# Performance work log

Measured on AMD Instinct MI355X. Metric: run time of the kernel, lower is better.

## Reference

```python
import jax, jax.numpy as jnp
import numpy as np

NT, NB, NC = 64, 1024, 512
H, E, NCLS = 512, 128, 97


def gru_cell(x, h, w_ih, w_hh, b_ih, b_hh):
    # torch.nn.GRUCell semantics; gate order r, z, n
    gi = x @ w_ih.T + b_ih
    gh = h @ w_hh.T + b_hh
    ir, iz, inn = jnp.split(gi, 3, axis=1)
    hr, hz, hn = jnp.split(gh, 3, axis=1)
    r = jax.nn.sigmoid(ir + hr)
    z = jax.nn.sigmoid(iz + hz)
    n = jnp.tanh(inn + r * hn)
    return (1.0 - z) * n + z * h


def setup_inputs() -> dict:
    key = jax.random.key(0)
    ks = jax.random.split(key, 12)
    s = 0.02
    return {
        'feats': jax.random.normal(ks[0], (NT, NB, NC), jnp.float32),
        'w_i2h': jax.random.normal(ks[1], (H, NC), jnp.float32) * s,
        'w_h2h': jax.random.normal(ks[2], (H, H), jnp.float32) * s,
        'b_h2h': jnp.zeros((H,), jnp.float32),
        'w_score': jax.random.normal(ks[3], (1, H), jnp.float32) * s,
        'w_ih': jax.random.normal(ks[4], (3 * H, NC + E), jnp.float32) * s,
        'w_hh': jax.random.normal(ks[5], (3 * H, H), jnp.float32) * s,
        'b_ih': jnp.zeros((3 * H,), jnp.float32),
        'b_hh': jnp.zeros((3 * H,), jnp.float32),
        'char_emb': jax.random.normal(ks[6], (NCLS + 1, E), jnp.float32),
        'w_gen': jax.random.normal(ks[7], (NCLS, H), jnp.float32) * s,
        'b_gen': jnp.zeros((NCLS,), jnp.float32),
        'text_length': jax.random.randint(ks[8], (NB,), 1, 33),
    }


def reference(feats, w_i2h, w_h2h, b_h2h, w_score, w_ih, w_hh, b_ih, b_hh,
              char_emb, w_gen, b_gen, text_length):
    # Attention.forward with test=True (greedy decode)
    nT, nB, nC = feats.shape
    tl = np.asarray(text_length)
    num_steps = int(tl.max())

    # i2h(feats) is identical every step -> hoist out of the loop
    feats_proj = jnp.einsum('tbc,hc->tbh', feats, w_i2h)  # [T,B,H]

    def step(carry, _):
        hidden, tgt = carry  # hidden [B,H], tgt [B] int
        hproj = hidden @ w_h2h.T + b_h2h                     # [B,H]
        e = jnp.tanh(feats_proj + hproj[None]) @ w_score[0]  # [T,B]
        alpha = jax.nn.softmax(e, axis=0)                    # softmax over nT
        context = jnp.einsum('tbc,tb->bc', feats, alpha)     # [B,C]
        x = jnp.concatenate([context, char_emb[tgt]], axis=1)  # [B,C+E]
        new_hidden = gru_cell(x, hidden, w_ih, w_hh, b_ih, b_hh)
        logits = new_hidden @ w_gen.T + b_gen                # [B,NCLS]
        new_tgt = jnp.argmax(logits, axis=1) + 1
        return (new_hidden, new_tgt), logits

    h0 = jnp.zeros((nB, w_h2h.shape[0]), feats.dtype)
    t0 = jnp.zeros((nB,), jnp.int32)
    _, probs = jax.lax.scan(step, (h0, t0), None, length=num_steps)  # [S,B,NCLS]
    probs = probs.transpose(1, 0, 2)  # [B,S,NCLS]

    # ragged gather: first text_length[b] steps of each batch element
    b_idx = np.repeat(np.arange(nB), tl)
    t_idx = np.concatenate([np.arange(l) for l in tl])
    return probs[b_idx, t_idx]  # [num_labels, NCLS]
```

## Files before the change

kernel.cpp:

```cpp
#include <hip/hip_runtime.h>
#include <math.h>

#define NT 64
#define NB 1024
#define NC 512
#define HH 512
#define EE 128
#define NCLS 97
#define STEPS 32

#define LDSW 80

typedef __bf16 bf16_t;
typedef bf16_t bf16x8 __attribute__((ext_vector_type(8)));
typedef float f32x4 __attribute__((ext_vector_type(4)));
typedef unsigned short u16x8 __attribute__((ext_vector_type(8)));

__device__ __forceinline__ float fast_tanh(float x) {
  float e = __expf(2.f * x);
  return 1.f - 2.f / (e + 1.f);
}
__device__ __forceinline__ float fast_sig(float x) {
  return 1.f / (1.f + __expf(-x));
}

__device__ __forceinline__ unsigned short bf16_rne(float x) {
  unsigned u = __float_as_uint(x);
  unsigned r = u + 0x7FFFu + ((u >> 16) & 1u);
  return (unsigned short)(r >> 16);
}
__device__ __forceinline__ void split2(float x, unsigned short& h,
                                       unsigned short& l) {
  unsigned u = __float_as_uint(x);
  h = (unsigned short)(u >> 16);
  float hf = __uint_as_float(u & 0xFFFF0000u);
  l = bf16_rne(x - hf);
}

__global__ __launch_bounds__(256) void gemm_mfma_big(
    const float* __restrict__ A, const unsigned short* __restrict__ Bhg,
    const unsigned short* __restrict__ Blg, float* __restrict__ C, int N,
    int K) {
  __shared__ __attribute__((aligned(16))) char Ah[128 * LDSW];
  __shared__ __attribute__((aligned(16))) char Al[128 * LDSW];
  __shared__ __attribute__((aligned(16))) char Bh[128 * LDSW];
  __shared__ __attribute__((aligned(16))) char Bl[128 * LDSW];
  const int bm = blockIdx.y * 128;
  const int bn = blockIdx.x * 128;
  const int tid = threadIdx.x;
  const int sr = tid >> 1;
  const int sq = (tid & 1) * 16;
  const int lane = tid & 63, wid = tid >> 6;
  const int wm = (wid >> 1) * 64, wn = (wid & 1) * 64;
  const int lr = lane & 15;
  const int ks = (lane >> 4) * 16;

  const float* Ap = A + (size_t)(bm + sr) * K + sq;
  const unsigned short* Bph = Bhg + (size_t)(bn + sr) * K + sq;
  const unsigned short* Bpl = Blg + (size_t)(bn + sr) * K + sq;

  f32x4 acc[4][4];
  f32x4 z;
  z[0] = 0.f; z[1] = 0.f; z[2] = 0.f; z[3] = 0.f;
#pragma unroll
  for (int i = 0; i < 4; ++i)
#pragma unroll
    for (int j = 0; j < 4; ++j) acc[i][j] = z;

  float4 pa[4];
  u16x8 pbh[2], pbl[2];
#pragma unroll
  for (int f = 0; f < 4; ++f) pa[f] = *(const float4*)(Ap + f * 4);
#pragma unroll
  for (int g = 0; g < 2; ++g) {
    pbh[g] = *(const u16x8*)(Bph + g * 8);
    pbl[g] = *(const u16x8*)(Bpl + g * 8);
  }

  for (int k0 = 0; k0 < K; k0 += 32) {
#pragma unroll
    for (int f = 0; f < 4; ++f) {
      ushort4 h4, l4;
      split2(pa[f].x, h4.x, l4.x);
      split2(pa[f].y, h4.y, l4.y);
      split2(pa[f].z, h4.z, l4.z);
      split2(pa[f].w, h4.w, l4.w);
      int off = sr * LDSW + sq * 2 + f * 8;
      *(ushort4*)(Ah + off) = h4;
      *(ushort4*)(Al + off) = l4;
    }
#pragma unroll
    for (int g = 0; g < 2; ++g) {
      int off = sr * LDSW + sq * 2 + g * 16;
      *(u16x8*)(Bh + off) = pbh[g];
      *(u16x8*)(Bl + off) = pbl[g];
    }
    __syncthreads();
    if (k0 + 32 < K) {
#pragma unroll
      for (int f = 0; f < 4; ++f)
        pa[f] = *(const float4*)(Ap + k0 + 32 + f * 4);
#pragma unroll
      for (int g = 0; g < 2; ++g) {
        pbh[g] = *(const u16x8*)(Bph + k0 + 32 + g * 8);
        pbl[g] = *(const u16x8*)(Bpl + k0 + 32 + g * 8);
      }
    }
    bf16x8 a_h[4], a_l[4], b_h[4], b_l[4];
#pragma unroll
    for (int mf = 0; mf < 4; ++mf) {
      int ro = (wm + mf * 16 + lr) * LDSW + ks;
      a_h[mf] = *(const bf16x8*)(Ah + ro);
      a_l[mf] = *(const bf16x8*)(Al + ro);
    }
#pragma unroll
    for (int nf = 0; nf < 4; ++nf) {
      int ro = (wn + nf * 16 + lr) * LDSW + ks;
      b_h[nf] = *(const bf16x8*)(Bh + ro);
      b_l[nf] = *(const bf16x8*)(Bl + ro);
    }
#pragma unroll
    for (int mf = 0; mf < 4; ++mf)
#pragma unroll
      for (int nf = 0; nf < 4; ++nf)
        acc[mf][nf] = __builtin_amdgcn_mfma_f32_16x16x32_bf16(
            a_h[mf], b_h[nf], acc[mf][nf], 0, 0, 0);
#pragma unroll
    for (int mf = 0; mf < 4; ++mf)
#pragma unroll
      for (int nf = 0; nf < 4; ++nf)
        acc[mf][nf] = __builtin_amdgcn_mfma_f32_16x16x32_bf16(
            a_h[mf], b_l[nf], acc[mf][nf], 0, 0, 0);
#pragma unroll
    for (int mf = 0; mf < 4; ++mf)
#pragma unroll
      for (int nf = 0; nf < 4; ++nf)
        acc[mf][nf] = __builtin_amdgcn_mfma_f32_16x16x32_bf16(
            a_l[mf], b_h[nf], acc[mf][nf], 0, 0, 0);
    __syncthreads();
  }
#pragma unroll
  for (int mf = 0; mf < 4; ++mf) {
    int row0 = bm + wm + mf * 16 + (lane >> 4) * 4;
#pragma unroll
    for (int nf = 0; nf < 4; ++nf) {
      int col = bn + wn + nf * 16 + lr;
      float* Cp = C + (size_t)row0 * N + col;
      Cp[0] = acc[mf][nf][0];
      Cp[N] = acc[mf][nf][1];
      Cp[2 * N] = acc[mf][nf][2];
      Cp[3 * N] = acc[mf][nf][3];
    }
  }
}

__global__ __launch_bounds__(256) void gemm_mfma_step(
    const float* __restrict__ A, int lda, const unsigned short* __restrict__ Bhg,
    const unsigned short* __restrict__ Blg, const float* __restrict__ bias,
    float* __restrict__ Ca, float* __restrict__ Cb, int ldc,
    const int* __restrict__ cnt, int step) {
  const int bm = blockIdx.y * 64;
  if (bm >= cnt[step]) return;
  __shared__ __attribute__((aligned(16))) char Ah[64 * LDSW];
  __shared__ __attribute__((aligned(16))) char Al[64 * LDSW];
  __shared__ __attribute__((aligned(16))) char Bh[128 * LDSW];
  __shared__ __attribute__((aligned(16))) char Bl[128 * LDSW];
  const int kh = blockIdx.z;
  const int kbase = kh * 256;
  float* __restrict__ C = kh ? Cb : Ca;
  const int bn = blockIdx.x * 128;
  const int tid = threadIdx.x;
  const int ar = tid >> 2, aq = (tid & 3) * 8;
  const int br = tid >> 1, bq = (tid & 1) * 16;
  const int lane = tid & 63, wid = tid >> 6;
  const int wm = (wid >> 1) * 32, wn = (wid & 1) * 64;
  const int lr = lane & 15;
  const int ks = (lane >> 4) * 16;

  const float* Ap = A + (size_t)(bm + ar) * lda + kbase + aq;
  const unsigned short* Bph = Bhg + (size_t)(bn + br) * 512 + kbase + bq;
  const unsigned short* Bpl = Blg + (size_t)(bn + br) * 512 + kbase + bq;

  f32x4 acc[2][4];
  f32x4 z;
  z[0] = 0.f; z[1] = 0.f; z[2] = 0.f; z[3] = 0.f;
#pragma unroll
  for (int i = 0; i < 2; ++i)
#pragma unroll
    for (int j = 0; j < 4; ++j) acc[i][j] = z;

  float4 pa[2];
  u16x8 pbh[2], pbl[2];
  pa[0] = *(const float4*)(Ap);
  pa[1] = *(const float4*)(Ap + 4);
#pragma unroll
  for (int g = 0; g < 2; ++g) {
    pbh[g] = *(const u16x8*)(Bph + g * 8);
    pbl[g] = *(const u16x8*)(Bpl + g * 8);
  }

  for (int k0 = 0; k0 < 256; k0 += 32) {
#pragma unroll
    for (int f = 0; f < 2; ++f) {
      ushort4 h4, l4;
      float4 v = pa[f];
      split2(v.x, h4.x, l4.x);
      split2(v.y, h4.y, l4.y);
      split2(v.z, h4.z, l4.z);
      split2(v.w, h4.w, l4.w);
      int off = ar * LDSW + aq * 2 + f * 8;
      *(ushort4*)(Ah + off) = h4;
      *(ushort4*)(Al + off) = l4;
    }
#pragma unroll
    for (int g = 0; g < 2; ++g) {
      int off = br * LDSW + bq * 2 + g * 16;
      *(u16x8*)(Bh + off) = pbh[g];
      *(u16x8*)(Bl + off) = pbl[g];
    }
    __syncthreads();
    if (k0 + 32 < 256) {
      pa[0] = *(const float4*)(Ap + k0 + 32);
      pa[1] = *(const float4*)(Ap + k0 + 36);
#pragma unroll
      for (int g = 0; g < 2; ++g) {
        pbh[g] = *(const u16x8*)(Bph + k0 + 32 + g * 8);
        pbl[g] = *(const u16x8*)(Bpl + k0 + 32 + g * 8);
      }
    }
    bf16x8 a_h[2], a_l[2], b_h[4], b_l[4];
#pragma unroll
    for (int mf = 0; mf < 2; ++mf) {
      int ro = (wm + mf * 16 + lr) * LDSW + ks;
      a_h[mf] = *(const bf16x8*)(Ah + ro);
      a_l[mf] = *(const bf16x8*)(Al + ro);
    }
#pragma unroll
    for (int nf = 0; nf < 4; ++nf) {
      int ro = (wn + nf * 16 + lr) * LDSW + ks;
      b_h[nf] = *(const bf16x8*)(Bh + ro);
      b_l[nf] = *(const bf16x8*)(Bl + ro);
    }
#pragma unroll
    for (int mf = 0; mf < 2; ++mf)
#pragma unroll
      for (int nf = 0; nf < 4; ++nf)
        acc[mf][nf] = __builtin_amdgcn_mfma_f32_16x16x32_bf16(
            a_h[mf], b_h[nf], acc[mf][nf], 0, 0, 0);
#pragma unroll
    for (int mf = 0; mf < 2; ++mf)
#pragma unroll
      for (int nf = 0; nf < 4; ++nf)
        acc[mf][nf] = __builtin_amdgcn_mfma_f32_16x16x32_bf16(
            a_h[mf], b_l[nf], acc[mf][nf], 0, 0, 0);
#pragma unroll
    for (int mf = 0; mf < 2; ++mf)
#pragma unroll
      for (int nf = 0; nf < 4; ++nf)
        acc[mf][nf] = __builtin_amdgcn_mfma_f32_16x16x32_bf16(
            a_l[mf], b_h[nf], acc[mf][nf], 0, 0, 0);
    __syncthreads();
  }
  float bc[4] = {0.f, 0.f, 0.f, 0.f};
  if (bias && kh == 0) {
#pragma unroll
    for (int nf = 0; nf < 4; ++nf) bc[nf] = bias[bn + wn + nf * 16 + lr];
  }
#pragma unroll
  for (int mf = 0; mf < 2; ++mf) {
    int row0 = bm + wm + mf * 16 + (lane >> 4) * 4;
#pragma unroll
    for (int nf = 0; nf < 4; ++nf) {
      int col = bn + wn + nf * 16 + lr;
      float* Cp = C + (size_t)row0 * ldc + col;
      Cp[0] = acc[mf][nf][0] + bc[nf];
      Cp[ldc] = acc[mf][nf][1] + bc[nf];
      Cp[2 * ldc] = acc[mf][nf][2] + bc[nf];
      Cp[3 * ldc] = acc[mf][nf][3] + bc[nf];
    }
  }
}

__global__ __launch_bounds__(512) void step_attn2(
    const float* __restrict__ fp, const float* __restrict__ C1a,
    const float* __restrict__ C1b, const float* __restrict__ w_score,
    const float* __restrict__ feats, float* __restrict__ context,
    const int* __restrict__ perm, const int* __restrict__ cnt, int step) {
  const int i0 = blockIdx.x;
  if (i0 >= cnt[step]) return;
  __shared__ float es[NT];
  __shared__ float als[NT];
  const int b = perm[i0];
  const int tid = threadIdx.x;
  const int lane = tid & 63, wid = tid >> 6;
  const float* hpa = C1a + (size_t)i0 * 2048 + lane * 8;
  const float* hpb = C1b + (size_t)i0 * 2048 + lane * 8;
  float4 ha0 = *(const float4*)hpa;
  float4 ha1 = *(const float4*)(hpa + 4);
  float4 hb0 = *(const float4*)hpb;
  float4 hb1 = *(const float4*)(hpb + 4);
  float4 h0, h1;
  h0.x = ha0.x + hb0.x; h0.y = ha0.y + hb0.y;
  h0.z = ha0.z + hb0.z; h0.w = ha0.w + hb0.w;
  h1.x = ha1.x + hb1.x; h1.y = ha1.y + hb1.y;
  h1.z = ha1.z + hb1.z; h1.w = ha1.w + hb1.w;
  float4 w0 = *(const float4*)(w_score + lane * 8);
  float4 w1 = *(const float4*)(w_score + lane * 8 + 4);
#pragma unroll
  for (int pass = 0; pass < 2; ++pass) {
    float4 f0[4], f1[4];
#pragma unroll
    for (int i = 0; i < 4; ++i) {
      int t = wid * 8 + pass * 4 + i;
      const float* fr = fp + ((size_t)t * NB + b) * HH + lane * 8;
      f0[i] = *(const float4*)fr;
      f1[i] = *(const float4*)(fr + 4);
    }
#pragma unroll
    for (int i = 0; i < 4; ++i) {
      float acc = 0.f;
      acc += fast_tanh(f0[i].x + h0.x) * w0.x;
      acc += fast_tanh(f0[i].y + h0.y) * w0.y;
      acc += fast_tanh(f0[i].z + h0.z) * w0.z;
      acc += fast_tanh(f0[i].w + h0.w) * w0.w;
      acc += fast_tanh(f1[i].x + h1.x) * w1.x;
      acc += fast_tanh(f1[i].y + h1.y) * w1.y;
      acc += fast_tanh(f1[i].z + h1.z) * w1.z;
      acc += fast_tanh(f1[i].w + h1.w) * w1.w;
#pragma unroll
      for (int off = 32; off > 0; off >>= 1) acc += __shfl_down(acc, off, 64);
      if (lane == 0) es[wid * 8 + pass * 4 + i] = acc;
    }
  }
  __syncthreads();
  if (tid < 64) {
    float v = es[tid];
    float mx = v;
#pragma unroll
    for (int off = 32; off > 0; off >>= 1) mx = fmaxf(mx, __shfl_xor(mx, off, 64));
    float p = __expf(v - mx);
    float sum = p;
#pragma unroll
    for (int off = 32; off > 0; off >>= 1) sum += __shfl_xor(sum, off, 64);
    als[tid] = p / sum;
  }
  __syncthreads();
  float a0 = 0.f, a1 = 0.f, a2 = 0.f, a3 = 0.f;
  const float* fb = feats + (size_t)b * NC + tid;
#pragma unroll 4
  for (int t = 0; t < NT; t += 4) {
    a0 += als[t + 0] * fb[(size_t)(t + 0) * NB * NC];
    a1 += als[t + 1] * fb[(size_t)(t + 1) * NB * NC];
    a2 += als[t + 2] * fb[(size_t)(t + 2) * NB * NC];
    a3 += als[t + 3] * fb[(size_t)(t + 3) * NB * NC];
  }
  context[(size_t)i0 * NC + tid] = ((a0 + a1) + (a2 + a3));
}

__global__ __launch_bounds__(128) void step_update2(
    const float* __restrict__ C1a, const float* __restrict__ C1b,
    const float* __restrict__ Ga, const float* __restrict__ Gb,
    const float* __restrict__ P, const float* __restrict__ hc,
    float* __restrict__ hn_out, const float* __restrict__ w_gen,
    const float* __restrict__ b_gen, const int* __restrict__ offs,
    float* __restrict__ out, int* __restrict__ tgt,
    const int* __restrict__ perm, const int* __restrict__ cnt, int step) {
  const int i0 = blockIdx.x;
  if (i0 >= cnt[step]) return;
  __shared__ float hs[HH];
  __shared__ float lv[128];
  __shared__ int li[128];
  const int b = perm[i0];
  const int tid = threadIdx.x;
  const int tg = tgt[b];
  const float* gia = Ga + (size_t)i0 * 1536;
  const float* gib = Gb + (size_t)i0 * 1536;
  const float* Pb = P + (size_t)tg * 1536;
  const float* gha = C1a + (size_t)i0 * 2048 + 512;
  const float* ghb = C1b + (size_t)i0 * 2048 + 512;
#pragma unroll
  for (int i = 0; i < 4; ++i) {
    int j = tid + i * 128;
    float ir = gia[j] + gib[j] + Pb[j];
    float iz = gia[512 + j] + gib[512 + j] + Pb[512 + j];
    float in = gia[1024 + j] + gib[1024 + j] + Pb[1024 + j];
    float hr = gha[j] + ghb[j];
    float hz = gha[512 + j] + ghb[512 + j];
    float hnv = gha[1024 + j] + ghb[1024 + j];
    float r = fast_sig(ir + hr);
    float z = fast_sig(iz + hz);
    float n = fast_tanh(in + r * hnv);
    float h = hc[(size_t)i0 * HH + j];
    float hv = (1.f - z) * n + z * h;
    hs[j] = hv;
    hn_out[(size_t)i0 * HH + j] = hv;
  }
  __syncthreads();
  float acc = -INFINITY;
  if (tid < NCLS) {
    const float4* wr4 = (const float4*)(w_gen + (size_t)tid * HH);
    float s = 0.f;
    for (int k = 0; k < HH / 4; ++k) {
      float4 w = wr4[k];
      s += hs[4 * k + 0] * w.x + hs[4 * k + 1] * w.y +
           hs[4 * k + 2] * w.z + hs[4 * k + 3] * w.w;
    }
    acc = s + b_gen[tid];
    out[(size_t)(offs[b] + step) * NCLS + tid] = acc;
  }
  lv[tid] = acc;
  li[tid] = tid;
  __syncthreads();
  for (int d = 64; d > 0; d >>= 1) {
    if (tid < d) {
      float v2 = lv[tid + d];
      int i2 = li[tid + d];
      if (v2 > lv[tid] || (v2 == lv[tid] && i2 < li[tid])) {
        lv[tid] = v2;
        li[tid] = i2;
      }
    }
    __syncthreads();
  }
  if (tid == 0) tgt[b] = li[0] + 1;
}

__global__ __launch_bounds__(1024) void sort_tl(const int* __restrict__ tl,
                                                int* __restrict__ perm,
                                                int* __restrict__ cnt,
                                                int* __restrict__ offs) {
  __shared__ int s[NB];
  const int t = threadIdx.x;
  s[t] = tl[t];
  __syncthreads();
  const int myv = s[t];
  int pos = 0;
  int pre = 0;
  for (int b = 0; b < NB; ++b) {
    int v = s[b];
    pos += (v > myv || (v == myv && b < t)) ? 1 : 0;
    pre += (b < t) ? v : 0;
  }
  perm[pos] = t;
  offs[t] = pre;
  if (t < STEPS) {
    int c = 0;
    for (int b = 0; b < NB; ++b) c += (s[b] > t) ? 1 : 0;
    cnt[t] = c;
  }
}

__global__ __launch_bounds__(256) void build_P(
    const float* __restrict__ char_emb, const float* __restrict__ w_ih,
    const float* __restrict__ b_ih, float* __restrict__ P) {
  __shared__ float emb[EE];
  int c = blockIdx.x;
  int tid = threadIdx.x;
  if (tid < EE) emb[tid] = char_emb[c * EE + tid];
  __syncthreads();
  for (int j = tid; j < 3 * HH; j += 256) {
    const float* wr = w_ih + (size_t)j * (NC + EE) + NC;
    float s = 0.f;
    for (int k = 0; k < EE; ++k) s += emb[k] * wr[k];
    P[(size_t)c * 1536 + j] = s + b_ih[j];
  }
}

__global__ __launch_bounds__(256) void build_wcat(
    const float* __restrict__ w_h2h, const float* __restrict__ w_hh,
    const float* __restrict__ b_h2h, const float* __restrict__ b_hh,
    float* __restrict__ Wcat, float* __restrict__ bcat) {
  int idx = blockIdx.x * 256 + threadIdx.x;
  const int n1 = 512 * 512 / 4;
  float4* dst = (float4*)Wcat;
  if (idx < n1)
    dst[idx] = ((const float4*)w_h2h)[idx];
  else
    dst[idx] = ((const float4*)w_hh)[idx - n1];
  if (idx < 2048) bcat[idx] = (idx < 512) ? b_h2h[idx] : b_hh[idx - 512];
}

__global__ __launch_bounds__(256) void split512(
    const float* __restrict__ src, int ld, unsigned short* __restrict__ hi,
    unsigned short* __restrict__ lo, int rows) {
  int idx = blockIdx.x * 256 + threadIdx.x;
  if (idx >= rows * 512) return;
  int r = idx >> 9, c = idx & 511;
  float x = src[(size_t)r * ld + c];
  unsigned short h, l;
  split2(x, h, l);
  hi[idx] = h;
  lo[idx] = l;
}

__global__ __launch_bounds__(256) void init_kernel(float* __restrict__ h0,
                                                   int* __restrict__ tgt) {
  int idx = blockIdx.x * 256 + threadIdx.x;
  if (idx < NB * HH) h0[idx] = 0.f;
  if (idx < NB) tgt[idx] = 0;
}

extern "C" void kernel_launch(void* const* d_in, const int* in_sizes, int n_in,
                              void* d_out, int out_size, void* d_ws,
                              size_t ws_size, hipStream_t stream) {
  const float* feats = (const float*)d_in[0];
  const float* w_i2h = (const float*)d_in[1];
  const float* w_h2h = (const float*)d_in[2];
  const float* b_h2h = (const float*)d_in[3];
  const float* w_score = (const float*)d_in[4];
  const float* w_ih = (const float*)d_in[5];
  const float* w_hh = (const float*)d_in[6];
  const float* b_ih = (const float*)d_in[7];
  const float* b_hh = (const float*)d_in[8];
  const float* char_emb = (const float*)d_in[9];
  const float* w_gen = (const float*)d_in[10];
  const float* b_gen = (const float*)d_in[11];
  const int* tl = (const int*)d_in[12];
  float* out = (float*)d_out;

  char* ws = (char*)d_ws;
  float* fp = (float*)ws;      ws += (size_t)NT * NB * HH * 4;
  float* C1a = (float*)ws;     ws += (size_t)NB * 2048 * 4;
  float* C1b = (float*)ws;     ws += (size_t)NB * 2048 * 4;
  float* Ga = (float*)ws;      ws += (size_t)NB * 1536 * 4;
  float* Gb = (float*)ws;      ws += (size_t)NB * 1536 * 4;
  float* context = (float*)ws; ws += (size_t)NB * NC * 4;
  float* h0 = (float*)ws;      ws += (size_t)NB * HH * 4;
  float* h1 = (float*)ws;      ws += (size_t)NB * HH * 4;
  float* Wcat = (float*)ws;    ws += (size_t)2048 * 512 * 4;
  float* bcat = (float*)ws;    ws += 2048 * 4;
  float* P = (float*)ws;       ws += (size_t)98 * 1536 * 4;
  unsigned short* Wi_h = (unsigned short*)ws; ws += (size_t)512 * 512 * 2;
  unsigned short* Wi_l = (unsigned short*)ws; ws += (size_t)512 * 512 * 2;
  unsigned short* Wc_h = (unsigned short*)ws; ws += (size_t)2048 * 512 * 2;
  unsigned short* Wc_l = (unsigned short*)ws; ws += (size_t)2048 * 512 * 2;
  unsigned short* Wg_h = (unsigned short*)ws; ws += (size_t)1536 * 512 * 2;
  unsigned short* Wg_l = (unsigned short*)ws; ws += (size_t)1536 * 512 * 2;
  int* tgt = (int*)ws;         ws += 4096;
  int* offs = (int*)ws;        ws += 4096;
  int* perm = (int*)ws;        ws += 4096;
  int* cnt = (int*)ws;         ws += 4096;

  hipLaunchKernelGGL(sort_tl, dim3(1), dim3(1024), 0, stream, tl, perm, cnt,
                     offs);
  hipLaunchKernelGGL(init_kernel, dim3((NB * HH) / 256), dim3(256), 0, stream,
                     h0, tgt);
  hipLaunchKernelGGL(build_wcat, dim3(1024), dim3(256), 0, stream, w_h2h, w_hh,
                     b_h2h, b_hh, Wcat, bcat);
  hipLaunchKernelGGL(build_P, dim3(98), dim3(256), 0, stream, char_emb, w_ih,
                     b_ih, P);
  hipLaunchKernelGGL(split512, dim3(512 * 2), dim3(256), 0, stream, w_i2h, 512,
                     Wi_h, Wi_l, 512);
  hipLaunchKernelGGL(split512, dim3(2048 * 2), dim3(256), 0, stream, Wcat, 512,
                     Wc_h, Wc_l, 2048);
  hipLaunchKernelGGL(split512, dim3(1536 * 2), dim3(256), 0, stream, w_ih, 640,
                     Wg_h, Wg_l, 1536);
  hipLaunchKernelGGL(gemm_mfma_big, dim3(HH / 128, (NT * NB) / 128), dim3(256),
                     0, stream, feats, Wi_h, Wi_l, fp, HH, NC);

  float* hbuf[2] = {h0, h1};
  for (int s = 0; s < STEPS; ++s) {
    float* hc = hbuf[s & 1];
    float* hn = hbuf[(s + 1) & 1];
    hipLaunchKernelGGL(gemm_mfma_step, dim3(2048 / 128, NB / 64, 2), dim3(256),
                       0, stream, hc, HH, Wc_h, Wc_l, bcat, C1a, C1b, 2048,
                       cnt, s);
    hipLaunchKernelGGL(step_attn2, dim3(NB), dim3(512), 0, stream, fp, C1a,
                       C1b, w_score, feats, context, perm, cnt, s);
    hipLaunchKernelGGL(gemm_mfma_step, dim3(1536 / 128, NB / 64, 2), dim3(256),
                       0, stream, context, NC, Wg_h, Wg_l,
                       (const float*)nullptr, Ga, Gb, 1536, cnt, s);
    hipLaunchKernelGGL(step_update2, dim3(NB), dim3(128), 0, stream, C1a, C1b,
                       Ga, Gb, P, hc, hn, w_gen, b_gen, offs, out, tgt, perm,
                       cnt, s);
  }
}
```

Before: 2.672 ms.

## Drop split-K in step GEMMs, remap big GEMM blocks per XCD, widen LDS stores

```diff
diff --git a/kernel.cpp b/kernel.cpp
--- a/kernel.cpp
+++ b/kernel.cpp
@@ -45,8 +45,10 @@
   __shared__ __attribute__((aligned(16))) char Al[128 * LDSW];
   __shared__ __attribute__((aligned(16))) char Bh[128 * LDSW];
   __shared__ __attribute__((aligned(16))) char Bl[128 * LDSW];
-  const int bm = blockIdx.y * 128;
-  const int bn = blockIdx.x * 128;
+  const int bid = blockIdx.x;
+  const int xcd = bid & 7, idx = bid >> 3;
+  const int bm = (xcd * 64 + (idx >> 2)) * 128;
+  const int bn = (idx & 3) * 128;
   const int tid = threadIdx.x;
   const int sr = tid >> 1;
   const int sq = (tid & 1) * 16;
@@ -78,16 +80,20 @@
   }
 
   for (int k0 = 0; k0 < K; k0 += 32) {
-#pragma unroll
-    for (int f = 0; f < 4; ++f) {
-      ushort4 h4, l4;
-      split2(pa[f].x, h4.x, l4.x);
-      split2(pa[f].y, h4.y, l4.y);
-      split2(pa[f].z, h4.z, l4.z);
-      split2(pa[f].w, h4.w, l4.w);
-      int off = sr * LDSW + sq * 2 + f * 8;
-      *(ushort4*)(Ah + off) = h4;
-      *(ushort4*)(Al + off) = l4;
+    {
+      unsigned short hh[16], ll[16];
+#pragma unroll
+      for (int f = 0; f < 4; ++f) {
+        split2(pa[f].x, hh[f * 4 + 0], ll[f * 4 + 0]);
+        split2(pa[f].y, hh[f * 4 + 1], ll[f * 4 + 1]);
+        split2(pa[f].z, hh[f * 4 + 2], ll[f * 4 + 2]);
+        split2(pa[f].w, hh[f * 4 + 3], ll[f * 4 + 3]);
+      }
+      int off = sr * LDSW + sq * 2;
+      *(u16x8*)(Ah + off) = *(const u16x8*)&hh[0];
+      *(u16x8*)(Ah + off + 16) = *(const u16x8*)&hh[8];
+      *(u16x8*)(Al + off) = *(const u16x8*)&ll[0];
+      *(u16x8*)(Al + off + 16) = *(const u16x8*)&ll[8];
     }
 #pragma unroll
     for (int g = 0; g < 2; ++g) {
@@ -157,17 +163,13 @@
 __global__ __launch_bounds__(256) void gemm_mfma_step(
     const float* __restrict__ A, int lda, const unsigned short* __restrict__ Bhg,
     const unsigned short* __restrict__ Blg, const float* __restrict__ bias,
-    float* __restrict__ Ca, float* __restrict__ Cb, int ldc,
-    const int* __restrict__ cnt, int step) {
+    float* __restrict__ C, int ldc, const int* __restrict__ cnt, int step) {
   const int bm = blockIdx.y * 64;
   if (bm >= cnt[step]) return;
   __shared__ __attribute__((aligned(16))) char Ah[64 * LDSW];
   __shared__ __attribute__((aligned(16))) char Al[64 * LDSW];
   __shared__ __attribute__((aligned(16))) char Bh[128 * LDSW];
   __shared__ __attribute__((aligned(16))) char Bl[128 * LDSW];
-  const int kh = blockIdx.z;
-  const int kbase = kh * 256;
-  float* __restrict__ C = kh ? Cb : Ca;
   const int bn = blockIdx.x * 128;
   const int tid = threadIdx.x;
   const int ar = tid >> 2, aq = (tid & 3) * 8;
@@ -177,9 +179,9 @@
   const int lr = lane & 15;
   const int ks = (lane >> 4) * 16;
 
-  const float* Ap = A + (size_t)(bm + ar) * lda + kbase + aq;
-  const unsigned short* Bph = Bhg + (size_t)(bn + br) * 512 + kbase + bq;
-  const unsigned short* Bpl = Blg + (size_t)(bn + br) * 512 + kbase + bq;
+  const float* Ap = A + (size_t)(bm + ar) * lda + aq;
+  const unsigned short* Bph = Bhg + (size_t)(bn + br) * 512 + bq;
+  const unsigned short* Bpl = Blg + (size_t)(bn + br) * 512 + bq;
 
   f32x4 acc[2][4];
   f32x4 z;
@@ -199,18 +201,20 @@
     pbl[g] = *(const u16x8*)(Bpl + g * 8);
   }
 
-  for (int k0 = 0; k0 < 256; k0 += 32) {
-#pragma unroll
-    for (int f = 0; f < 2; ++f) {
-      ushort4 h4, l4;
-      float4 v = pa[f];
-      split2(v.x, h4.x, l4.x);
-      split2(v.y, h4.y, l4.y);
-      split2(v.z, h4.z, l4.z);
-      split2(v.w, h4.w, l4.w);
-      int off = ar * LDSW + aq * 2 + f * 8;
-      *(ushort4*)(Ah + off) = h4;
-      *(ushort4*)(Al + off) = l4;
+  for (int k0 = 0; k0 < 512; k0 += 32) {
+    {
+      unsigned short hh[8], ll[8];
+      split2(pa[0].x, hh[0], ll[0]);
+      split2(pa[0].y, hh[1], ll[1]);
+      split2(pa[0].z, hh[2], ll[2]);
+      split2(pa[0].w, hh[3], ll[3]);
+      split2(pa[1].x, hh[4], ll[4]);
+      split2(pa[1].y, hh[5], ll[5]);
+      split2(pa[1].z, hh[6], ll[6]);
+      split2(pa[1].w, hh[7], ll[7]);
+      int off = ar * LDSW + aq * 2;
+      *(u16x8*)(Ah + off) = *(const u16x8*)&hh[0];
+      *(u16x8*)(Al + off) = *(const u16x8*)&ll[0];
     }
 #pragma unroll
     for (int g = 0; g < 2; ++g) {
@@ -219,7 +223,7 @@
       *(u16x8*)(Bl + off) = pbl[g];
     }
     __syncthreads();
-    if (k0 + 32 < 256) {
+    if (k0 + 32 < 512) {
       pa[0] = *(const float4*)(Ap + k0 + 32);
       pa[1] = *(const float4*)(Ap + k0 + 36);
 #pragma unroll
@@ -262,7 +266,7 @@
     __syncthreads();
   }
   float bc[4] = {0.f, 0.f, 0.f, 0.f};
-  if (bias && kh == 0) {
+  if (bias) {
 #pragma unroll
     for (int nf = 0; nf < 4; ++nf) bc[nf] = bias[bn + wn + nf * 16 + lr];
   }
@@ -282,10 +286,10 @@
 }
 
 __global__ __launch_bounds__(512) void step_attn2(
-    const float* __restrict__ fp, const float* __restrict__ C1a,
-    const float* __restrict__ C1b, const float* __restrict__ w_score,
-    const float* __restrict__ feats, float* __restrict__ context,
-    const int* __restrict__ perm, const int* __restrict__ cnt, int step) {
+    const float* __restrict__ fp, const float* __restrict__ C1,
+    const float* __restrict__ w_score, const float* __restrict__ feats,
+    float* __restrict__ context, const int* __restrict__ perm,
+    const int* __restrict__ cnt, int step) {
   const int i0 = blockIdx.x;
   if (i0 >= cnt[step]) return;
   __shared__ float es[NT];
@@ -293,17 +297,9 @@
   const int b = perm[i0];
   const int tid = threadIdx.x;
   const int lane = tid & 63, wid = tid >> 6;
-  const float* hpa = C1a + (size_t)i0 * 2048 + lane * 8;
-  const float* hpb = C1b + (size_t)i0 * 2048 + lane * 8;
-  float4 ha0 = *(const float4*)hpa;
-  float4 ha1 = *(const float4*)(hpa + 4);
-  float4 hb0 = *(const float4*)hpb;
-  float4 hb1 = *(const float4*)(hpb + 4);
-  float4 h0, h1;
-  h0.x = ha0.x + hb0.x; h0.y = ha0.y + hb0.y;
-  h0.z = ha0.z + hb0.z; h0.w = ha0.w + hb0.w;
-  h1.x = ha1.x + hb1.x; h1.y = ha1.y + hb1.y;
-  h1.z = ha1.z + hb1.z; h1.w = ha1.w + hb1.w;
+  const float* hp = C1 + (size_t)i0 * 2048 + lane * 8;
+  float4 h0 = *(const float4*)hp;
+  float4 h1 = *(const float4*)(hp + 4);
   float4 w0 = *(const float4*)(w_score + lane * 8);
   float4 w1 = *(const float4*)(w_score + lane * 8 + 4);
 #pragma unroll
@@ -358,8 +354,7 @@
 }
 
 __global__ __launch_bounds__(128) void step_update2(
-    const float* __restrict__ C1a, const float* __restrict__ C1b,
-    const float* __restrict__ Ga, const float* __restrict__ Gb,
+    const float* __restrict__ C1, const float* __restrict__ G,
     const float* __restrict__ P, const float* __restrict__ hc,
     float* __restrict__ hn_out, const float* __restrict__ w_gen,
     const float* __restrict__ b_gen, const int* __restrict__ offs,
@@ -373,20 +368,18 @@
   const int b = perm[i0];
   const int tid = threadIdx.x;
   const int tg = tgt[b];
-  const float* gia = Ga + (size_t)i0 * 1536;
-  const float* gib = Gb + (size_t)i0 * 1536;
+  const float* gi = G + (size_t)i0 * 1536;
   const float* Pb = P + (size_t)tg * 1536;
-  const float* gha = C1a + (size_t)i0 * 2048 + 512;
-  const float* ghb = C1b + (size_t)i0 * 2048 + 512;
+  const float* gh = C1 + (size_t)i0 * 2048 + 512;
 #pragma unroll
   for (int i = 0; i < 4; ++i) {
     int j = tid + i * 128;
-    float ir = gia[j] + gib[j] + Pb[j];
-    float iz = gia[512 + j] + gib[512 + j] + Pb[512 + j];
-    float in = gia[1024 + j] + gib[1024 + j] + Pb[1024 + j];
-    float hr = gha[j] + ghb[j];
-    float hz = gha[512 + j] + ghb[512 + j];
-    float hnv = gha[1024 + j] + ghb[1024 + j];
+    float ir = gi[j] + Pb[j];
+    float iz = gi[512 + j] + Pb[512 + j];
+    float in = gi[1024 + j] + Pb[1024 + j];
+    float hr = gh[j];
+    float hz = gh[512 + j];
+    float hnv = gh[1024 + j];
     float r = fast_sig(ir + hr);
     float z = fast_sig(iz + hz);
     float n = fast_tanh(in + r * hnv);
@@ -520,10 +513,8 @@
 
   char* ws = (char*)d_ws;
   float* fp = (float*)ws;      ws += (size_t)NT * NB * HH * 4;
-  float* C1a = (float*)ws;     ws += (size_t)NB * 2048 * 4;
-  float* C1b = (float*)ws;     ws += (size_t)NB * 2048 * 4;
-  float* Ga = (float*)ws;      ws += (size_t)NB * 1536 * 4;
-  float* Gb = (float*)ws;      ws += (size_t)NB * 1536 * 4;
+  float* C1 = (float*)ws;      ws += (size_t)NB * 2048 * 4;
+  float* G = (float*)ws;       ws += (size_t)NB * 1536 * 4;
   float* context = (float*)ws; ws += (size_t)NB * NC * 4;
   float* h0 = (float*)ws;      ws += (size_t)NB * HH * 4;
   float* h1 = (float*)ws;      ws += (size_t)NB * HH * 4;
@@ -555,23 +546,21 @@
                      Wc_h, Wc_l, 2048);
   hipLaunchKernelGGL(split512, dim3(1536 * 2), dim3(256), 0, stream, w_ih, 640,
                      Wg_h, Wg_l, 1536);
-  hipLaunchKernelGGL(gemm_mfma_big, dim3(HH / 128, (NT * NB) / 128), dim3(256),
-                     0, stream, feats, Wi_h, Wi_l, fp, HH, NC);
+  hipLaunchKernelGGL(gemm_mfma_big, dim3(2048), dim3(256), 0, stream, feats,
+                     Wi_h, Wi_l, fp, HH, NC);
 
   float* hbuf[2] = {h0, h1};
   for (int s = 0; s < STEPS; ++s) {
     float* hc = hbuf[s & 1];
     float* hn = hbuf[(s + 1) & 1];
-    hipLaunchKernelGGL(gemm_mfma_step, dim3(2048 / 128, NB / 64, 2), dim3(256),
-                       0, stream, hc, HH, Wc_h, Wc_l, bcat, C1a, C1b, 2048,
-                       cnt, s);
-    hipLaunchKernelGGL(step_attn2, dim3(NB), dim3(512), 0, stream, fp, C1a,
-                       C1b, w_score, feats, context, perm, cnt, s);
-    hipLaunchKernelGGL(gemm_mfma_step, dim3(1536 / 128, NB / 64, 2), dim3(256),
-                       0, stream, context, NC, Wg_h, Wg_l,
-                       (const float*)nullptr, Ga, Gb, 1536, cnt, s);
-    hipLaunchKernelGGL(step_update2, dim3(NB), dim3(128), 0, stream, C1a, C1b,
-                       Ga, Gb, P, hc, hn, w_gen, b_gen, offs, out, tgt, perm,
-                       cnt, s);
-  }
-}
+    hipLaunchKernelGGL(gemm_mfma_step, dim3(2048 / 128, NB / 64), dim3(256), 0,
+                       stream, hc, HH, Wc_h, Wc_l, bcat, C1, 2048, cnt, s);
+    hipLaunchKernelGGL(step_attn2, dim3(NB), dim3(512), 0, stream, fp, C1,
+                       w_score, feats, context, perm, cnt, s);
+    hipLaunchKernelGGL(gemm_mfma_step, dim3(1536 / 128, NB / 64), dim3(256), 0,
+                       stream, context, NC, Wg_h, Wg_l,
+                       (const float*)nullptr, G, 1536, cnt, s);
+    hipLaunchKernelGGL(step_update2, dim3(NB), dim3(128), 0, stream, C1, G, P,
+                       hc, hn, w_gen, b_gen, offs, out, tgt, perm, cnt, s);
+  }
+}
```

Measured after the change: 3.032 ms. 1.13x slower.
